# Performance work log

Measured on AMD Instinct MI355X. Metric: run time of the kernel, lower is better.

Reference implementation:

```python
import jax, jax.numpy as jnp
import numpy as np

D_MODEL = 1024
NUM_HEADS = 16
DEPTH = D_MODEL // NUM_HEADS


def setup_inputs() -> dict:
    key = jax.random.key(0)
    ks = jax.random.split(key, 11)
    B, S = 2, 2048
    scale = 0.02
    inp = {
        "queries": jax.random.normal(ks[0], (B, S, D_MODEL), jnp.float32),
        "keys": jax.random.normal(ks[1], (B, S, D_MODEL), jnp.float32),
        "values": jax.random.normal(ks[2], (B, S, D_MODEL), jnp.float32),
        "wq": jax.random.normal(ks[3], (D_MODEL, D_MODEL), jnp.float32) * scale,
        "bq": jnp.zeros((D_MODEL,), jnp.float32),
        "wk": jax.random.normal(ks[4], (D_MODEL, D_MODEL), jnp.float32) * scale,
        "bk": jnp.zeros((D_MODEL,), jnp.float32),
        "wv": jax.random.normal(ks[5], (D_MODEL, D_MODEL), jnp.float32) * scale,
        "bv": jnp.zeros((D_MODEL,), jnp.float32),
        "wo": jax.random.normal(ks[6], (D_MODEL, D_MODEL), jnp.float32) * scale,
        "bo": jnp.zeros((D_MODEL,), jnp.float32),
    }
    return inp


def _split_heads(x):
    # [B, S, D] -> [B, H, S, depth]
    B, S, _ = x.shape
    return x.reshape(B, S, NUM_HEADS, DEPTH).transpose(0, 2, 1, 3)


def reference(queries, keys, values, wq, bq, wk, bk, wv, bv, wo, bo):
    B, S, _ = queries.shape
    q = _split_heads(queries @ wq + bq)  # [B,H,S,d]
    k = _split_heads(keys @ wk + bk)
    v = _split_heads(values @ wv + bv)
    dk = jnp.asarray(DEPTH, jnp.float32)
    scores = jnp.einsum("bhqd,bhkd->bhqk", q, k) / jnp.sqrt(dk)
    weights = jax.nn.softmax(scores, axis=-1)  # [B,H,S,S]
    attn = jnp.einsum("bhqk,bhkd->bhqd", weights, v)
    concat = attn.transpose(0, 2, 1, 3).reshape(B, S, D_MODEL)
    out = concat @ wo + bo
    return (out, weights)
```

## Files before the change

### kernel.cpp

```cpp
#include <hip/hip_runtime.h>
#include <hip/hip_bf16.h>

#define DM 1024
#define S_LEN 2048
#define NH 16
#define DEPTH 64
#define BATCH 2
#define LOG2E 1.4426950408889634f

typedef float f32x4 __attribute__((ext_vector_type(4)));
typedef __bf16 bf16x8 __attribute__((ext_vector_type(8)));
typedef unsigned short us8 __attribute__((ext_vector_type(8)));
typedef unsigned short us4 __attribute__((ext_vector_type(4)));

__device__ __forceinline__ unsigned short b16(float f) {
  return __builtin_bit_cast(unsigned short, (__bf16)f);
}
__device__ __forceinline__ float ex2(float x) {
#if __has_builtin(__builtin_amdgcn_exp2f)
  return __builtin_amdgcn_exp2f(x);
#else
  return exp2f(x);
#endif
}
__device__ __forceinline__ f32x4 mfma16(us8 a, us8 b, f32x4 c) {
  return __builtin_amdgcn_mfma_f32_16x16x32_bf16(
      __builtin_bit_cast(bf16x8, a), __builtin_bit_cast(bf16x8, b), c, 0, 0, 0);
}
__device__ __forceinline__ void gll16(const void* g, void* l) {
  __builtin_amdgcn_global_load_lds(
      (const __attribute__((address_space(1))) void*)g,
      (__attribute__((address_space(3))) void*)l, 16, 0, 0);
}
#define SWZ_RD(baseB, r, c) \
  (*(const us8*)((baseB) + (size_t)(r) * 128 + ((((c) ^ ((r) & 7))) << 4)))

template <int RSB>
__device__ __forceinline__ void stage128(const char* Gb, int r0, int kb,
                                         char* dst, int tid) {
#pragma unroll
  for (int i = 0; i < 4; i++) {
    int t16 = i * 256 + tid;
    int row = t16 >> 3;
    int g = (t16 & 7) ^ (row & 7);
    gll16(Gb + (size_t)(r0 + row) * RSB + kb + (g << 4),
          dst + i * 4096 + (tid & ~63) * 16);
  }
}

__device__ __forceinline__ void stage64a(const char* Gb, int r0, int kb,
                                         char* dst, int tid) {
#pragma unroll
  for (int i = 0; i < 2; i++) {
    int t16 = i * 256 + tid;
    int row = t16 >> 3;
    int g = (t16 & 7) ^ (row & 7);
    gll16(Gb + (size_t)(r0 + row) * 2048 + kb + (g << 4),
          dst + i * 4096 + (tid & ~63) * 16);
  }
}

__device__ __forceinline__ void stage128k(const char* Gb, int r0, char* dst,
                                          int tid) {
#pragma unroll
  for (int i = 0; i < 4; i++) {
    int t16 = i * 256 + tid;
    int row = t16 >> 3;
    int g = (t16 & 7) ^ (row & 7);
    int i5 = row & 31, jj = i5 & 15, hi = i5 >> 4;
    int prow = (row & 96) | ((jj >> 2) << 3) | (hi << 2) | (jj & 3);
    gll16(Gb + (size_t)(r0 + prow) * 128 + (g << 4),
          dst + i * 4096 + (tid & ~63) * 16);
  }
}

__global__ __launch_bounds__(256) void prep_k(
    const float* __restrict__ q, const float* __restrict__ k,
    const float* __restrict__ v, unsigned short* __restrict__ oq,
    unsigned short* __restrict__ ok, unsigned short* __restrict__ ov,
    const float* __restrict__ w0, const float* __restrict__ w1,
    const float* __restrict__ w2, const float* __restrict__ w3,
    unsigned short* __restrict__ t0, unsigned short* __restrict__ t1,
    unsigned short* __restrict__ t2, unsigned short* __restrict__ t3) {
  const int y = blockIdx.y;
  if (y < 3) {
    const float* src = y == 0 ? q : y == 1 ? k : v;
    unsigned short* dst = y == 0 ? oq : y == 1 ? ok : ov;
    size_t i = ((size_t)blockIdx.x * 256 + threadIdx.x) * 8;
    float4 f0 = *(const float4*)(src + i);
    float4 f1 = *(const float4*)(src + i + 4);
    us8 o;
    o[0] = b16(f0.x); o[1] = b16(f0.y); o[2] = b16(f0.z); o[3] = b16(f0.w);
    o[4] = b16(f1.x); o[5] = b16(f1.y); o[6] = b16(f1.z); o[7] = b16(f1.w);
    *(us8*)(dst + i) = o;
  } else {
    if (blockIdx.x >= 1024) return;
    const int z = y - 3;
    const float* W = z == 0 ? w0 : z == 1 ? w1 : z == 2 ? w2 : w3;
    unsigned short* Wt = z == 0 ? t0 : z == 1 ? t1 : z == 2 ? t2 : t3;
    __shared__ float tile[32][33];
    const int ti = blockIdx.x >> 5, tj = blockIdx.x & 31;
    const int c = threadIdx.x & 31, r8 = threadIdx.x >> 5;
#pragma unroll
    for (int i = 0; i < 4; i++) {
      int r = r8 * 4 + i;
      tile[r][c] = W[(size_t)(ti * 32 + r) * DM + tj * 32 + c];
    }
    __syncthreads();
#pragma unroll
    for (int i = 0; i < 4; i++) {
      int r = r8 * 4 + i;
      Wt[(size_t)(tj * 32 + r) * DM + ti * 32 + c] = b16(tile[c][r]);
    }
  }
}

__device__ __forceinline__ void gemm_mainloop64(const char* Ab, const char* Bb,
    char* AsB, char* BsB, int m0, int n0, int tid, int t0,
    f32x4 (&acc)[2][4]) {
  const int lane = tid & 63, w = tid >> 6;
  const int ln = lane & 15, lh = lane >> 4;
  const int wr = w >> 1, wc = w & 1;
  stage64a(Ab, m0, t0 * 128, AsB, tid);
  stage128<2048>(Bb, n0, t0 * 128, BsB, tid);
  __syncthreads();
  for (int i = 0; i < 16; i++) {
    const int curA = (i & 1) << 13, curB = (i & 1) << 14;
    if (i < 15) {
      const int kb = ((t0 + i + 1) & 15) * 128;
      stage64a(Ab, m0, kb, AsB + (curA ^ (1 << 13)), tid);
      stage128<2048>(Bb, n0, kb, BsB + (curB ^ (1 << 14)), tid);
    }
#pragma unroll
    for (int ks = 0; ks < 2; ks++) {
      us8 af[2], bf[4];
#pragma unroll
      for (int mi = 0; mi < 2; mi++)
        af[mi] = SWZ_RD(AsB + curA, wr * 32 + mi * 16 + ln, ks * 4 + lh);
#pragma unroll
      for (int c = 0; c < 4; c++)
        bf[c] = SWZ_RD(BsB + curB, wc * 64 + c * 16 + ln, ks * 4 + lh);
#pragma unroll
      for (int mi = 0; mi < 2; mi++)
#pragma unroll
        for (int c = 0; c < 4; c++)
          acc[mi][c] = mfma16(af[mi], bf[c], acc[mi][c]);
    }
    __syncthreads();
  }
}

__global__ __launch_bounds__(256) void gemm_qkv_k(
    const unsigned short* __restrict__ Aq, const unsigned short* __restrict__ Ak,
    const unsigned short* __restrict__ Av, const unsigned short* __restrict__ Wq,
    const unsigned short* __restrict__ Wk, const unsigned short* __restrict__ Wv,
    const float* __restrict__ bq, const float* __restrict__ bk,
    const float* __restrict__ bv, unsigned short* __restrict__ oq,
    unsigned short* __restrict__ ok, unsigned short* __restrict__ ov,
    float qscale) {
  __shared__ unsigned short As[2 * 64 * 64];
  __shared__ unsigned short Bs[2 * 128 * 64];
  const int z = blockIdx.z;
  const unsigned short* A = z == 0 ? Aq : z == 1 ? Ak : Av;
  const unsigned short* Wt = z == 0 ? Wq : z == 1 ? Wk : Wv;
  const float* bias = z == 0 ? bq : z == 1 ? bk : bv;
  unsigned short* out = z == 0 ? oq : z == 1 ? ok : ov;
  const float scale = z == 0 ? qscale : 1.0f;
  const int m0 = blockIdx.x * 64, n0 = blockIdx.y * 128;
  const int tid = threadIdx.x, lane = tid & 63, w = tid >> 6;
  const int ln = lane & 15, lh = lane >> 4;
  const int wr = w >> 1, wc = w & 1;
  const int t0 = (blockIdx.x * 7 + blockIdx.y * 3 + blockIdx.z) & 15;
  f32x4 acc[2][4] = {};
  gemm_mainloop64((const char*)A, (const char*)Wt, (char*)As, (char*)Bs,
                  m0, n0, tid, t0, acc);
#pragma unroll
  for (int mi = 0; mi < 2; mi++) {
#pragma unroll
    for (int c = 0; c < 4; c++) {
      const int n = n0 + wc * 64 + c * 16 + ln;
      const float bv_ = bias[n];
      const int h = n >> 6, d = n & 63;
      const int mbase = m0 + wr * 32 + mi * 16 + lh * 4;
      if (z < 2) {
#pragma unroll
        for (int r = 0; r < 4; r++) {
          int m = mbase + r, b = m >> 11, s = m & (S_LEN - 1);
          out[((size_t)(b * NH + h) * S_LEN + s) * DEPTH + d] =
              b16((acc[mi][c][r] + bv_) * scale);
        }
      } else {
        const int b = mbase >> 11, s = mbase & (S_LEN - 1);
        us4 pk;
#pragma unroll
        for (int r = 0; r < 4; r++) pk[r] = b16(acc[mi][c][r] + bv_);
        *(us4*)&out[((size_t)(b * NH + h) * DEPTH + d) * S_LEN + s] = pk;
      }
    }
  }
}

__global__ __launch_bounds__(256) void gemm_out_k(
    const unsigned short* __restrict__ A, const unsigned short* __restrict__ Wt,
    const float* __restrict__ bias, float* __restrict__ out) {
  __shared__ unsigned short As[2 * 64 * 64];
  __shared__ unsigned short Bs[2 * 128 * 64];
  const int m0 = blockIdx.x * 64, n0 = blockIdx.y * 128;
  const int tid = threadIdx.x, lane = tid & 63, w = tid >> 6;
  const int ln = lane & 15, lh = lane >> 4;
  const int wr = w >> 1, wc = w & 1;
  const int t0 = (blockIdx.x * 7 + blockIdx.y * 3) & 15;
  f32x4 acc[2][4] = {};
  gemm_mainloop64((const char*)A, (const char*)Wt, (char*)As, (char*)Bs,
                  m0, n0, tid, t0, acc);
#pragma unroll
  for (int mi = 0; mi < 2; mi++) {
#pragma unroll
    for (int c = 0; c < 4; c++) {
      const int n = n0 + wc * 64 + c * 16 + ln;
      const float bv_ = bias[n];
      const int mbase = m0 + wr * 32 + mi * 16 + lh * 4;
#pragma unroll
      for (int r = 0; r < 4; r++)
        out[(size_t)(mbase + r) * DM + n] = acc[mi][c][r] + bv_;
    }
  }
}

__global__ __launch_bounds__(256) void attn_k(const unsigned short* __restrict__ Qh,
    const unsigned short* __restrict__ Kh, const unsigned short* __restrict__ Vt,
    float* __restrict__ Wout, unsigned short* __restrict__ attnOut) {
  __shared__ unsigned short Ks[2 * 128 * 64];
  char* KsB = (char*)Ks;
  const int flat = blockIdx.x;
  const int xcd = flat & 7, g = flat >> 3;
  const int qt = g & 31;
  const int bh = xcd + 8 * (g >> 5);
  const int tid = threadIdx.x, w = tid >> 6, lane = tid & 63;
  const int ln = lane & 15, lh = lane >> 4;
  const int q0 = qt * 64;
  const unsigned short* Qb = Qh + (size_t)bh * S_LEN * DEPTH;
  const char* KbB = (const char*)(Kh + (size_t)bh * S_LEN * DEPTH);
  const unsigned short* Vb = Vt + (size_t)bh * DEPTH * S_LEN;
  const int qrow = q0 + w * 16 + ln;
  const us8 qf0 = *(const us8*)(Qb + (size_t)qrow * DEPTH + lh * 8);
  const us8 qf1 = *(const us8*)(Qb + (size_t)qrow * DEPTH + 32 + lh * 8);

  float l = 0.f;
  stage128k(KbB, 0, KsB, tid);
  __syncthreads();
  for (int t = 0; t < 16; t++) {
    const int cur = (t & 1) << 14, nxt = cur ^ (1 << 14);
    if (t < 15) stage128k(KbB, (t + 1) * 128, KsB + nxt, tid);
#pragma unroll
    for (int kt2 = 0; kt2 < 4; kt2++) {
      const int r0 = kt2 * 32 + ln;
      f32x4 d0 = {0.f, 0.f, 0.f, 0.f}, d1 = {0.f, 0.f, 0.f, 0.f};
      d0 = mfma16(SWZ_RD(KsB + cur, r0, lh), qf0, d0);
      d0 = mfma16(SWZ_RD(KsB + cur, r0, 4 + lh), qf1, d0);
      d1 = mfma16(SWZ_RD(KsB + cur, r0 + 16, lh), qf0, d1);
      d1 = mfma16(SWZ_RD(KsB + cur, r0 + 16, 4 + lh), qf1, d1);
      l += (ex2(d0[0]) + ex2(d0[1])) + (ex2(d0[2]) + ex2(d0[3])) +
           (ex2(d1[0]) + ex2(d1[1])) + (ex2(d1[2]) + ex2(d1[3]));
    }
    __syncthreads();
  }
  l += __shfl_xor(l, 16);
  l += __shfl_xor(l, 32);
  const float rl = 1.0f / l;

  f32x4 o[4] = {};
  float* Wr = Wout + (size_t)bh * S_LEN * S_LEN + (size_t)(q0 + w * 16 + ln) * S_LEN;
  const int t0 = qt & 15;
  stage128k(KbB, t0 * 128, KsB, tid);
  __syncthreads();
  for (int i = 0; i < 16; i++) {
    const int t = (t0 + i) & 15;
    const int cur = (i & 1) << 14, nxt = cur ^ (1 << 14);
    if (i < 15) stage128k(KbB, ((t0 + i + 1) & 15) * 128, KsB + nxt, tid);
    __builtin_amdgcn_sched_barrier(0);
    const int sc = t * 128;
#pragma unroll
    for (int kt2 = 0; kt2 < 4; kt2++) {
      const int r0 = kt2 * 32 + ln;
      f32x4 d0 = {0.f, 0.f, 0.f, 0.f}, d1 = {0.f, 0.f, 0.f, 0.f};
      d0 = mfma16(SWZ_RD(KsB + cur, r0, lh), qf0, d0);
      d0 = mfma16(SWZ_RD(KsB + cur, r0, 4 + lh), qf1, d0);
      d1 = mfma16(SWZ_RD(KsB + cur, r0 + 16, lh), qf0, d1);
      d1 = mfma16(SWZ_RD(KsB + cur, r0 + 16, 4 + lh), qf1, d1);
      f32x4 w0, w1;
#pragma unroll
      for (int r = 0; r < 4; r++) {
        w0[r] = ex2(d0[r]) * rl;
        w1[r] = ex2(d1[r]) * rl;
      }
      *(f32x4*)(Wr + sc + kt2 * 32 + 8 * lh) = w0;
      *(f32x4*)(Wr + sc + kt2 * 32 + 8 * lh + 4) = w1;
      us8 af;
      af[0] = b16(w0[0]); af[1] = b16(w0[1]);
      af[2] = b16(w0[2]); af[3] = b16(w0[3]);
      af[4] = b16(w1[0]); af[5] = b16(w1[1]);
      af[6] = b16(w1[2]); af[7] = b16(w1[3]);
#pragma unroll
      for (int dt = 0; dt < 4; dt++) {
        us8 vf = *(const us8*)(Vb + (size_t)(dt * 16 + ln) * S_LEN + sc +
                               kt2 * 32 + lh * 8);
        o[dt] = mfma16(af, vf, o[dt]);
      }
    }
    asm volatile("s_waitcnt vmcnt(8)" ::: "memory");
    __builtin_amdgcn_s_barrier();
  }

  const int b = bh >> 4, h = bh & 15;
#pragma unroll
  for (int dt = 0; dt < 4; dt++) {
#pragma unroll
    for (int r = 0; r < 4; r++) {
      size_t row = (size_t)b * S_LEN + q0 + w * 16 + lh * 4 + r;
      attnOut[row * DM + h * DEPTH + dt * 16 + ln] = b16(o[dt][r]);
    }
  }
}

extern "C" void kernel_launch(void* const* d_in, const int* in_sizes, int n_in,
                              void* d_out, int out_size, void* d_ws, size_t ws_size,
                              hipStream_t stream) {
  const float* queries = (const float*)d_in[0];
  const float* keys    = (const float*)d_in[1];
  const float* values  = (const float*)d_in[2];
  const float* wq = (const float*)d_in[3];
  const float* bq = (const float*)d_in[4];
  const float* wk = (const float*)d_in[5];
  const float* bk = (const float*)d_in[6];
  const float* wv = (const float*)d_in[7];
  const float* bv = (const float*)d_in[8];
  const float* wo = (const float*)d_in[9];
  const float* bo = (const float*)d_in[10];

  float* out = (float*)d_out;
  float* wts = out + (size_t)BATCH * S_LEN * DM;

  char* ws = (char*)d_ws;
  const size_t WSZ = (size_t)DM * DM * sizeof(unsigned short);
  const size_t TSZ = (size_t)BATCH * S_LEN * DM * sizeof(unsigned short);
  unsigned short* Wqt = (unsigned short*)(ws + 0 * WSZ);
  unsigned short* Wkt = (unsigned short*)(ws + 1 * WSZ);
  unsigned short* Wvt = (unsigned short*)(ws + 2 * WSZ);
  unsigned short* Wot = (unsigned short*)(ws + 3 * WSZ);
  unsigned short* Qbf = (unsigned short*)(ws + 4 * WSZ + 0 * TSZ);
  unsigned short* Kbf = (unsigned short*)(ws + 4 * WSZ + 1 * TSZ);
  unsigned short* Vbf = (unsigned short*)(ws + 4 * WSZ + 2 * TSZ);
  unsigned short* Qhd = (unsigned short*)(ws + 4 * WSZ + 3 * TSZ);
  unsigned short* Khd = (unsigned short*)(ws + 4 * WSZ + 4 * TSZ);
  unsigned short* Vtd = (unsigned short*)(ws + 4 * WSZ + 5 * TSZ);
  unsigned short* attn = Qbf;

  prep_k<<<dim3(2048, 7), 256, 0, stream>>>(queries, keys, values,
                                            Qbf, Kbf, Vbf,
                                            wq, wk, wv, wo,
                                            Wqt, Wkt, Wvt, Wot);
  gemm_qkv_k<<<dim3(64, 8, 3), 256, 0, stream>>>(Qbf, Kbf, Vbf, Wqt, Wkt, Wvt,
                                                 bq, bk, bv, Qhd, Khd, Vtd,
                                                 0.125f * LOG2E);
  attn_k<<<1024, 256, 0, stream>>>(Qhd, Khd, Vtd, wts, attn);
  gemm_out_k<<<dim3(64, 8), 256, 0, stream>>>(attn, Wot, bo, out);
}
```

Measured before the change: 268.9 us.

## Split softmax row-sum pass into separate kernel processing 128 query rows per block

Moves the first attention pass (computing softmax denominators) into its own kernel in which each block handles 128 query rows, so every K tile staged in shared memory feeds twice as many MFMAs. The reciprocal row sums go to a workspace buffer that the second-pass kernel reads. This halves K reloads for the denominator pass, at the cost of an extra kernel launch, a small global write and read, and a grid of 512 blocks that may leave CUs underused.

```diff
diff --git a/kernel.cpp b/kernel.cpp
--- a/kernel.cpp
+++ b/kernel.cpp
@@ -227,8 +227,66 @@
   }
 }
 
-__global__ __launch_bounds__(256) void attn_k(const unsigned short* __restrict__ Qh,
-    const unsigned short* __restrict__ Kh, const unsigned short* __restrict__ Vt,
+__global__ __launch_bounds__(256) void attn_p1_k(
+    const unsigned short* __restrict__ Qh, const unsigned short* __restrict__ Kh,
+    float* __restrict__ rlws) {
+  __shared__ unsigned short Ks[2 * 128 * 64];
+  char* KsB = (char*)Ks;
+  const int flat = blockIdx.x;
+  const int xcd = flat & 7, g = flat >> 3;
+  const int qt16 = g & 15;
+  const int bh = xcd + 8 * (g >> 4);
+  const int tid = threadIdx.x, w = tid >> 6, lane = tid & 63;
+  const int ln = lane & 15, lh = lane >> 4;
+  const int q0 = qt16 * 128;
+  const unsigned short* Qb = Qh + (size_t)bh * S_LEN * DEPTH;
+  const char* KbB = (const char*)(Kh + (size_t)bh * S_LEN * DEPTH);
+  const int ra = q0 + w * 16 + ln;
+  const int rb = ra + 64;
+  const us8 qa0 = *(const us8*)(Qb + (size_t)ra * DEPTH + lh * 8);
+  const us8 qa1 = *(const us8*)(Qb + (size_t)ra * DEPTH + 32 + lh * 8);
+  const us8 qb0 = *(const us8*)(Qb + (size_t)rb * DEPTH + lh * 8);
+  const us8 qb1 = *(const us8*)(Qb + (size_t)rb * DEPTH + 32 + lh * 8);
+
+  float la = 0.f, lb = 0.f;
+  stage128k(KbB, 0, KsB, tid);
+  __syncthreads();
+  for (int t = 0; t < 16; t++) {
+    const int cur = (t & 1) << 14, nxt = cur ^ (1 << 14);
+    if (t < 15) stage128k(KbB, (t + 1) * 128, KsB + nxt, tid);
+#pragma unroll
+    for (int kt2 = 0; kt2 < 4; kt2++) {
+      const int r0 = kt2 * 32 + ln;
+      const us8 k0 = SWZ_RD(KsB + cur, r0, lh);
+      const us8 k1 = SWZ_RD(KsB + cur, r0, 4 + lh);
+      const us8 k2 = SWZ_RD(KsB + cur, r0 + 16, lh);
+      const us8 k3 = SWZ_RD(KsB + cur, r0 + 16, 4 + lh);
+      f32x4 d0a = {0.f, 0.f, 0.f, 0.f}, d1a = {0.f, 0.f, 0.f, 0.f};
+      f32x4 d0b = {0.f, 0.f, 0.f, 0.f}, d1b = {0.f, 0.f, 0.f, 0.f};
+      d0a = mfma16(k0, qa0, d0a); d0a = mfma16(k1, qa1, d0a);
+      d1a = mfma16(k2, qa0, d1a); d1a = mfma16(k3, qa1, d1a);
+      d0b = mfma16(k0, qb0, d0b); d0b = mfma16(k1, qb1, d0b);
+      d1b = mfma16(k2, qb0, d1b); d1b = mfma16(k3, qb1, d1b);
+      la += (ex2(d0a[0]) + ex2(d0a[1])) + (ex2(d0a[2]) + ex2(d0a[3])) +
+            (ex2(d1a[0]) + ex2(d1a[1])) + (ex2(d1a[2]) + ex2(d1a[3]));
+      lb += (ex2(d0b[0]) + ex2(d0b[1])) + (ex2(d0b[2]) + ex2(d0b[3])) +
+            (ex2(d1b[0]) + ex2(d1b[1])) + (ex2(d1b[2]) + ex2(d1b[3]));
+    }
+    __syncthreads();
+  }
+  la += __shfl_xor(la, 16);
+  la += __shfl_xor(la, 32);
+  lb += __shfl_xor(lb, 16);
+  lb += __shfl_xor(lb, 32);
+  if (lh == 0) {
+    rlws[(size_t)bh * S_LEN + ra] = 1.0f / la;
+    rlws[(size_t)bh * S_LEN + rb] = 1.0f / lb;
+  }
+}
+
+__global__ __launch_bounds__(256) void attn_p2_k(
+    const unsigned short* __restrict__ Qh, const unsigned short* __restrict__ Kh,
+    const unsigned short* __restrict__ Vt, const float* __restrict__ rlws,
     float* __restrict__ Wout, unsigned short* __restrict__ attnOut) {
   __shared__ unsigned short Ks[2 * 128 * 64];
   char* KsB = (char*)Ks;
@@ -245,32 +303,10 @@
   const int qrow = q0 + w * 16 + ln;
   const us8 qf0 = *(const us8*)(Qb + (size_t)qrow * DEPTH + lh * 8);
   const us8 qf1 = *(const us8*)(Qb + (size_t)qrow * DEPTH + 32 + lh * 8);
-
-  float l = 0.f;
-  stage128k(KbB, 0, KsB, tid);
-  __syncthreads();
-  for (int t = 0; t < 16; t++) {
-    const int cur = (t & 1) << 14, nxt = cur ^ (1 << 14);
-    if (t < 15) stage128k(KbB, (t + 1) * 128, KsB + nxt, tid);
-#pragma unroll
-    for (int kt2 = 0; kt2 < 4; kt2++) {
-      const int r0 = kt2 * 32 + ln;
-      f32x4 d0 = {0.f, 0.f, 0.f, 0.f}, d1 = {0.f, 0.f, 0.f, 0.f};
-      d0 = mfma16(SWZ_RD(KsB + cur, r0, lh), qf0, d0);
-      d0 = mfma16(SWZ_RD(KsB + cur, r0, 4 + lh), qf1, d0);
-      d1 = mfma16(SWZ_RD(KsB + cur, r0 + 16, lh), qf0, d1);
-      d1 = mfma16(SWZ_RD(KsB + cur, r0 + 16, 4 + lh), qf1, d1);
-      l += (ex2(d0[0]) + ex2(d0[1])) + (ex2(d0[2]) + ex2(d0[3])) +
-           (ex2(d1[0]) + ex2(d1[1])) + (ex2(d1[2]) + ex2(d1[3]));
-    }
-    __syncthreads();
-  }
-  l += __shfl_xor(l, 16);
-  l += __shfl_xor(l, 32);
-  const float rl = 1.0f / l;
+  const float rl = rlws[(size_t)bh * S_LEN + qrow];
 
   f32x4 o[4] = {};
-  float* Wr = Wout + (size_t)bh * S_LEN * S_LEN + (size_t)(q0 + w * 16 + ln) * S_LEN;
+  float* Wr = Wout + (size_t)bh * S_LEN * S_LEN + (size_t)qrow * S_LEN;
   const int t0 = qt & 15;
   stage128k(KbB, t0 * 128, KsB, tid);
   __syncthreads();
@@ -354,6 +390,7 @@
   unsigned short* Qhd = (unsigned short*)(ws + 4 * WSZ + 3 * TSZ);
   unsigned short* Khd = (unsigned short*)(ws + 4 * WSZ + 4 * TSZ);
   unsigned short* Vtd = (unsigned short*)(ws + 4 * WSZ + 5 * TSZ);
+  float*          rlws = (float*)(ws + 4 * WSZ + 6 * TSZ);
   unsigned short* attn = Qbf;
 
   prep_k<<<dim3(2048, 7), 256, 0, stream>>>(queries, keys, values,
@@ -363,6 +400,7 @@
   gemm_qkv_k<<<dim3(64, 8, 3), 256, 0, stream>>>(Qbf, Kbf, Vbf, Wqt, Wkt, Wvt,
                                                  bq, bk, bv, Qhd, Khd, Vtd,
                                                  0.125f * LOG2E);
-  attn_k<<<1024, 256, 0, stream>>>(Qhd, Khd, Vtd, wts, attn);
+  attn_p1_k<<<512, 256, 0, stream>>>(Qhd, Khd, rlws);
+  attn_p2_k<<<1024, 256, 0, stream>>>(Qhd, Khd, Vtd, rlws, wts, attn);
   gemm_out_k<<<dim3(64, 8), 256, 0, stream>>>(attn, Wot, bo, out);
 }
```

Result: slower. 275.6 us (+2.5%).
